# Kernel optimization log

Measured on AMD Instinct MI355X. Metric: run time of the kernel, lower is better.

Reference implementation:

```python
import jax, jax.numpy as jnp
from jax import lax
import numpy as np

H = 16        # hidden_size == input_size
L = 8         # num_layers


def _lstm_layer(x_seq, Wih, Whh, bih, bhh):
    # x_seq: [B, T, H] -> outputs [B, T, H]; PyTorch gate order i,f,g,o
    B = x_seq.shape[0]
    b = bih + bhh  # [4H]

    def step(carry, xt):
        h, c = carry
        gates = xt @ Wih.T + h @ Whh.T + b  # [B, 4H]
        i, f, g, o = jnp.split(gates, 4, axis=-1)
        c = jax.nn.sigmoid(f) * c + jax.nn.sigmoid(i) * jnp.tanh(g)
        h = jax.nn.sigmoid(o) * jnp.tanh(c)
        return (h, c), h

    h0 = jnp.zeros((B, H), x_seq.dtype)
    (_, _), hs = lax.scan(step, (h0, h0), jnp.swapaxes(x_seq, 0, 1))
    return jnp.swapaxes(hs, 0, 1)  # [B, T, H]


def setup_inputs() -> dict:
    key = jax.random.key(0)
    ks = jax.random.split(key, 9)
    s = 1.0 / np.sqrt(H)  # PyTorch default init scale
    x = jax.random.normal(ks[0], (2048, 512, H), dtype=jnp.float32)
    W_ih = jax.random.uniform(ks[1], (L, 4 * H, H), jnp.float32, -s, s)
    W_hh = jax.random.uniform(ks[2], (L, 4 * H, H), jnp.float32, -s, s)
    b_ih = jax.random.uniform(ks[3], (L, 4 * H), jnp.float32, -s, s)
    b_hh = jax.random.uniform(ks[4], (L, 4 * H), jnp.float32, -s, s)
    Wp = jax.random.uniform(ks[5], (3, H), jnp.float32, -s, s)
    bp = jax.random.uniform(ks[6], (3,), jnp.float32, -s, s)
    Wo = jax.random.uniform(ks[7], (3, H), jnp.float32, -s, s)
    bo = jax.random.uniform(ks[8], (3,), jnp.float32, -s, s)
    return {"x": x, "W_ih": W_ih, "W_hh": W_hh, "b_ih": b_ih, "b_hh": b_hh,
            "Wp": Wp, "bp": bp, "Wo": Wo, "bo": bo}


def reference(x, W_ih, W_hh, b_ih, b_hh, Wp, bp, Wo, bo):
    h = x
    for l in range(L):  # fixed small layer count
        h = _lstm_layer(h, W_ih[l], W_hh[l], b_ih[l], b_hh[l])
    last = h[:, -1, :]                       # [B, H]
    position = last @ Wp.T + bp              # [B, 3]
    orientation = jnp.tanh(last @ Wo.T + bo) # [B, 3]
    return jnp.concatenate((position, orientation), axis=1)  # [B, 6]
```

## Files before the change

### kernel.cpp

```cpp
#include <hip/hip_runtime.h>
#include <math.h>

typedef _Float16 f16x4 __attribute__((ext_vector_type(4)));
typedef _Float16 f16x2 __attribute__((ext_vector_type(2)));
typedef float    f32x4 __attribute__((ext_vector_type(4)));

constexpr int kT      = 512;
constexpr int kH      = 16;
constexpr int kL      = 8;
constexpr int kNB     = 8;
constexpr int kC      = 16;
constexpr int kChunks = kT / kC;
constexpr int kStages = kChunks + kL - 1;
constexpr int kRowE   = kNB * kH;

constexpr float kL2E = 1.4426950408889634f;

__device__ __forceinline__ float ex2(float w)  { return __builtin_amdgcn_exp2f(w); }
__device__ __forceinline__ float rcpf(float e) { return __builtin_amdgcn_rcpf(e); }

__global__ __launch_bounds__(512, 2)
void lstm_ck(const float* __restrict__ x,
             const float* __restrict__ Wih, const float* __restrict__ Whh,
             const float* __restrict__ bih, const float* __restrict__ bhh,
             const float* __restrict__ Wp,  const float* __restrict__ bpos,
             const float* __restrict__ Wo,  const float* __restrict__ bori,
             float* __restrict__ out)
{
    const int tid  = threadIdx.x;
    const int l    = tid >> 6;
    const int lane = tid & 63;
    const int n    = lane & 15;
    const int q    = lane >> 4;
    const int b    = n & 7;
    const int hi   = n >> 3;

    __shared__ __align__(16) _Float16 hbuf[2][kL - 1][kC][kNB][kH];
    __shared__ __align__(16) _Float16 headb[kNB][kH];

    const float asc = ((n & 3) == 2) ? (-2.0f * kL2E) : (-kL2E);
    f16x4 A1[4], A2[4];
    f32x4 bias[4];
    #pragma unroll
    for (int p = 0; p < 4; ++p) {
        const int wrow = (n & 3) * 16 + 4 * (n >> 2) + p;
        const float* w1 = Wih + (size_t)l * 64 * kH + wrow * kH + 4 * q;
        const float* w2 = Whh + (size_t)l * 64 * kH + wrow * kH + 4 * q;
        #pragma unroll
        for (int jj = 0; jj < 4; ++jj) {
            A1[p][jj] = (_Float16)(asc * w1[jj]);
            A2[p][jj] = (_Float16)(asc * w2[jj]);
        }
        #pragma unroll
        for (int r = 0; r < 4; ++r) {
            const float sc = (r == 2) ? (-2.0f * kL2E) : (-kL2E);
            const int g0 = l * 64 + r * 16 + 4 * q + p;
            bias[p][r] = sc * (bih[g0] + bhh[g0]);
        }
    }

    const float* xg = x + ((size_t)(blockIdx.x * kNB + b) * kT) * kH + 4 * q;
    f32x4 xf[kC];
    if (l == 0) {
        #pragma unroll
        for (int j = 0; j < kC; ++j)
            xf[j] = *(const f32x4*)(xg + (size_t)j * kH);
    }

    f16x4 B2r = { (_Float16)0.f, (_Float16)0.f, (_Float16)0.f, (_Float16)0.f };
    float cA = 0.f, cB = 0.f;

    #pragma unroll 1
    for (int s = 0; s < kStages; ++s) {
        const int c = s - l;
        if ((unsigned)c < (unsigned)kChunks) {
            f16x4 B1f[kC];
            if (l == 0) {
                #pragma unroll
                for (int j = 0; j < kC; ++j) {
                    f16x4 v = { (_Float16)xf[j][0], (_Float16)xf[j][1],
                                (_Float16)xf[j][2], (_Float16)xf[j][3] };
                    B1f[j] = v;
                }
                if (c + 1 < kChunks) {
                    #pragma unroll
                    for (int j = 0; j < kC; ++j)
                        xf[j] = *(const f32x4*)(xg + (size_t)((c + 1) * kC + j) * kH);
                }
            } else {
                const _Float16* src = &hbuf[c & 1][l - 1][0][b][4 * q];
                #pragma unroll
                for (int j = 0; j < kC; ++j)
                    B1f[j] = *(const f16x4*)(src + j * kRowE);
            }

            _Float16* wdst = &hbuf[c & 1][(l < kL - 1) ? l : 0][0][b][4 * q + 2 * hi];

            #pragma unroll
            for (int j = 0; j < kC; ++j) {
                f32x4 dIn0 = __builtin_amdgcn_mfma_f32_16x16x16f16(A1[0], B1f[j], bias[0], 0, 0, 0);
                f32x4 dIn1 = __builtin_amdgcn_mfma_f32_16x16x16f16(A1[1], B1f[j], bias[1], 0, 0, 0);
                f32x4 dIn2 = __builtin_amdgcn_mfma_f32_16x16x16f16(A1[2], B1f[j], bias[2], 0, 0, 0);
                f32x4 dIn3 = __builtin_amdgcn_mfma_f32_16x16x16f16(A1[3], B1f[j], bias[3], 0, 0, 0);
                f32x4 d0 = __builtin_amdgcn_mfma_f32_16x16x16f16(A2[0], B2r, dIn0, 0, 0, 0);
                f32x4 d1 = __builtin_amdgcn_mfma_f32_16x16x16f16(A2[1], B2r, dIn1, 0, 0, 0);
                f32x4 d2 = __builtin_amdgcn_mfma_f32_16x16x16f16(A2[2], B2r, dIn2, 0, 0, 0);
                f32x4 d3 = __builtin_amdgcn_mfma_f32_16x16x16f16(A2[3], B2r, dIn3, 0, 0, 0);

                f32x4 dA, dB;
                #pragma unroll
                for (int r = 0; r < 4; ++r) {
                    dA[r] = hi ? d2[r] : d0[r];
                    dB[r] = hi ? d3[r] : d1[r];
                }

                float hAf, hBf;
                {
                    const float Ei = ex2(fminf(dA[0], 40.0f));
                    const float Ef = ex2(fminf(dA[1], 40.0f));
                    const float Eg = ex2(fminf(dA[2], 40.0f));
                    const float Eo = ex2(fminf(dA[3], 60.0f));
                    const float Dg = 1.0f + Eg;
                    const float Df = 1.0f + Ef;
                    const float P1  = fmaf(Ei, Dg, Dg);
                    const float den = Df * P1;
                    const float t2  = fmaf(-Eg, Df, Df);
                    const float num = fmaf(cA, P1, t2);
                    const float cn  = num * rcpf(den);
                    cA = cn;
                    const float ac = fminf(cn * (-2.0f * kL2E), 60.0f);
                    const float Ec = ex2(ac);
                    const float Do = 1.0f + Eo;
                    const float R2 = rcpf(fmaf(Do, Ec, Do));
                    hAf = fmaf(-Ec, R2, R2);
                }
                {
                    const float Ei = ex2(fminf(dB[0], 40.0f));
                    const float Ef = ex2(fminf(dB[1], 40.0f));
                    const float Eg = ex2(fminf(dB[2], 40.0f));
                    const float Eo = ex2(fminf(dB[3], 60.0f));
                    const float Dg = 1.0f + Eg;
                    const float Df = 1.0f + Ef;
                    const float P1  = fmaf(Ei, Dg, Dg);
                    const float den = Df * P1;
                    const float t2  = fmaf(-Eg, Df, Df);
                    const float num = fmaf(cB, P1, t2);
                    const float cn  = num * rcpf(den);
                    cB = cn;
                    const float ac = fminf(cn * (-2.0f * kL2E), 60.0f);
                    const float Ec = ex2(ac);
                    const float Do = 1.0f + Eo;
                    const float R2 = rcpf(fmaf(Do, Ec, Do));
                    hBf = fmaf(-Ec, R2, R2);
                }

                f16x2 hp = { (_Float16)hAf, (_Float16)hBf };
                union { f16x2 h; int i; } uh; uh.h = hp;
                const int own   = uh.i;
                const int other = __shfl_xor(own, 8, 64);
                union { int i2[2]; f16x4 v; } ub;
                ub.i2[0] = hi ? other : own;
                ub.i2[1] = hi ? own : other;
                B2r = ub.v;

                if (l < kL - 1)
                    *(f16x2*)(wdst + j * kRowE) = hp;
                if (l == kL - 1 && c == kChunks - 1 && j == kC - 1)
                    *(f16x2*)(&headb[b][4 * q + 2 * hi]) = hp;
            }
        }
        asm volatile("s_waitcnt lgkmcnt(0)\n\ts_barrier" ::: "memory");
    }

    __syncthreads();

    if (l == kL - 1) {
        const int bb = lane >> 3;
        const int r  = lane & 7;
        if (r < 6) {
            const bool  isP   = (r < 3);
            const float* wrow = isP ? (Wp + r * kH) : (Wo + (r - 3) * kH);
            float acc = isP ? bpos[r] : bori[r - 3];
            #pragma unroll
            for (int u = 0; u < kH; ++u)
                acc = fmaf((float)headb[bb][u], wrow[u], acc);
            if (!isP) {
                const float Et = ex2(-2.0f * kL2E * acc);
                acc = fmaf(2.0f, rcpf(1.0f + Et), -1.0f);
            }
            out[(size_t)(blockIdx.x * kNB + bb) * 6 + r] = acc;
        }
    }
}

extern "C" void kernel_launch(void* const* d_in, const int* in_sizes, int n_in,
                              void* d_out, int out_size, void* d_ws, size_t ws_size,
                              hipStream_t stream) {
    const float* x    = (const float*)d_in[0];
    const float* Wih  = (const float*)d_in[1];
    const float* Whh  = (const float*)d_in[2];
    const float* bih  = (const float*)d_in[3];
    const float* bhh  = (const float*)d_in[4];
    const float* Wp   = (const float*)d_in[5];
    const float* bpos = (const float*)d_in[6];
    const float* Wo   = (const float*)d_in[7];
    const float* bori = (const float*)d_in[8];
    float* out = (float*)d_out;

    const int B = in_sizes[0] / (kT * kH);
    lstm_ck<<<dim3(B / kNB), dim3(512), 0, stream>>>(x, Wih, Whh, bih, bhh,
                                                     Wp, bpos, Wo, bori, out);
}
```

Measured before the change: 308.2 us.

## Halve batch per block so each lane computes one hidden unit, doubling blocks

```diff
diff --git a/kernel.cpp b/kernel.cpp
--- a/kernel.cpp
+++ b/kernel.cpp
@@ -2,13 +2,13 @@
 #include <math.h>
 
 typedef _Float16 f16x4 __attribute__((ext_vector_type(4)));
-typedef _Float16 f16x2 __attribute__((ext_vector_type(2)));
 typedef float    f32x4 __attribute__((ext_vector_type(4)));
+typedef float    f32x2 __attribute__((ext_vector_type(2)));
 
 constexpr int kT      = 512;
 constexpr int kH      = 16;
 constexpr int kL      = 8;
-constexpr int kNB     = 8;
+constexpr int kNB     = 4;
 constexpr int kC      = 16;
 constexpr int kChunks = kT / kC;
 constexpr int kStages = kChunks + kL - 1;
@@ -19,21 +19,23 @@
 __device__ __forceinline__ float ex2(float w)  { return __builtin_amdgcn_exp2f(w); }
 __device__ __forceinline__ float rcpf(float e) { return __builtin_amdgcn_rcpf(e); }
 
-__global__ __launch_bounds__(512, 2)
-void lstm_ck(const float* __restrict__ x,
-             const float* __restrict__ Wih, const float* __restrict__ Whh,
-             const float* __restrict__ bih, const float* __restrict__ bhh,
-             const float* __restrict__ Wp,  const float* __restrict__ bpos,
-             const float* __restrict__ Wo,  const float* __restrict__ bori,
-             float* __restrict__ out)
+__global__ __launch_bounds__(512, 4)
+void lstm_ck4(const float* __restrict__ x,
+              const float* __restrict__ Wih, const float* __restrict__ Whh,
+              const float* __restrict__ bih, const float* __restrict__ bhh,
+              const float* __restrict__ Wp,  const float* __restrict__ bpos,
+              const float* __restrict__ Wo,  const float* __restrict__ bori,
+              float* __restrict__ out)
 {
     const int tid  = threadIdx.x;
     const int l    = tid >> 6;
     const int lane = tid & 63;
     const int n    = lane & 15;
     const int q    = lane >> 4;
-    const int b    = n & 7;
-    const int hi   = n >> 3;
+    const int b    = n & 3;
+    const int t4   = n >> 2;
+    const int p2   = t4 >> 1;
+    const int myU  = 4 * q + t4;
 
     __shared__ __align__(16) _Float16 hbuf[2][kL - 1][kC][kNB][kH];
     __shared__ __align__(16) _Float16 headb[kNB][kH];
@@ -59,122 +61,114 @@
         }
     }
 
-    const float* xg = x + ((size_t)(blockIdx.x * kNB + b) * kT) * kH + 4 * q;
-    f32x4 xf[kC];
+    const float* xg = x + ((size_t)(blockIdx.x * kNB + b) * kT) * kH
+                        + 4 * q + 2 * p2;
+    f32x2 xf[kC];
     if (l == 0) {
         #pragma unroll
         for (int j = 0; j < kC; ++j)
-            xf[j] = *(const f32x4*)(xg + (size_t)j * kH);
+            xf[j] = *(const f32x2*)(xg + (size_t)j * kH);
     }
 
     f16x4 B2r = { (_Float16)0.f, (_Float16)0.f, (_Float16)0.f, (_Float16)0.f };
-    float cA = 0.f, cB = 0.f;
+    float c0 = 0.f;
 
     #pragma unroll 1
     for (int s = 0; s < kStages; ++s) {
         const int c = s - l;
         if ((unsigned)c < (unsigned)kChunks) {
-            f16x4 B1f[kC];
-            if (l == 0) {
-                #pragma unroll
-                for (int j = 0; j < kC; ++j) {
-                    f16x4 v = { (_Float16)xf[j][0], (_Float16)xf[j][1],
-                                (_Float16)xf[j][2], (_Float16)xf[j][3] };
-                    B1f[j] = v;
-                }
-                if (c + 1 < kChunks) {
-                    #pragma unroll
-                    for (int j = 0; j < kC; ++j)
-                        xf[j] = *(const f32x4*)(xg + (size_t)((c + 1) * kC + j) * kH);
-                }
-            } else {
-                const _Float16* src = &hbuf[c & 1][l - 1][0][b][4 * q];
-                #pragma unroll
-                for (int j = 0; j < kC; ++j)
-                    B1f[j] = *(const f16x4*)(src + j * kRowE);
-            }
-
-            _Float16* wdst = &hbuf[c & 1][(l < kL - 1) ? l : 0][0][b][4 * q + 2 * hi];
+            const _Float16* rsrc = &hbuf[c & 1][(l > 0) ? (l - 1) : 0][0][b][4 * q];
+            _Float16* wdst = &hbuf[c & 1][(l < kL - 1) ? l : 0][0][b][myU];
+
+            auto xB1 = [&](int j) -> f16x4 {
+                union { _Float16 h[2]; int i; } up;
+                up.h[0] = (_Float16)xf[j][0];
+                up.h[1] = (_Float16)xf[j][1];
+                const int pd = up.i;
+                const int od = __shfl_xor(pd, 8, 64);
+                union { int i2[2]; f16x4 v; } ua;
+                ua.i2[0] = p2 ? od : pd;
+                ua.i2[1] = p2 ? pd : od;
+                return ua.v;
+            };
+
+            f16x4 B1cur;
+            if (l > 0) B1cur = *(const f16x4*)(rsrc);
+            else       B1cur = xB1(0);
 
             #pragma unroll
             for (int j = 0; j < kC; ++j) {
-                f32x4 dIn0 = __builtin_amdgcn_mfma_f32_16x16x16f16(A1[0], B1f[j], bias[0], 0, 0, 0);
-                f32x4 dIn1 = __builtin_amdgcn_mfma_f32_16x16x16f16(A1[1], B1f[j], bias[1], 0, 0, 0);
-                f32x4 dIn2 = __builtin_amdgcn_mfma_f32_16x16x16f16(A1[2], B1f[j], bias[2], 0, 0, 0);
-                f32x4 dIn3 = __builtin_amdgcn_mfma_f32_16x16x16f16(A1[3], B1f[j], bias[3], 0, 0, 0);
+                f16x4 B1nxt;
+                if (j < kC - 1) {
+                    if (l > 0) B1nxt = *(const f16x4*)(rsrc + (j + 1) * kRowE);
+                    else       B1nxt = xB1(j + 1);
+                }
+
+                f32x4 dIn0 = __builtin_amdgcn_mfma_f32_16x16x16f16(A1[0], B1cur, bias[0], 0, 0, 0);
+                f32x4 dIn1 = __builtin_amdgcn_mfma_f32_16x16x16f16(A1[1], B1cur, bias[1], 0, 0, 0);
+                f32x4 dIn2 = __builtin_amdgcn_mfma_f32_16x16x16f16(A1[2], B1cur, bias[2], 0, 0, 0);
+                f32x4 dIn3 = __builtin_amdgcn_mfma_f32_16x16x16f16(A1[3], B1cur, bias[3], 0, 0, 0);
                 f32x4 d0 = __builtin_amdgcn_mfma_f32_16x16x16f16(A2[0], B2r, dIn0, 0, 0, 0);
                 f32x4 d1 = __builtin_amdgcn_mfma_f32_16x16x16f16(A2[1], B2r, dIn1, 0, 0, 0);
                 f32x4 d2 = __builtin_amdgcn_mfma_f32_16x16x16f16(A2[2], B2r, dIn2, 0, 0, 0);
                 f32x4 d3 = __builtin_amdgcn_mfma_f32_16x16x16f16(A2[3], B2r, dIn3, 0, 0, 0);
 
-                f32x4 dA, dB;
+                f32x4 d;
                 #pragma unroll
                 for (int r = 0; r < 4; ++r) {
-                    dA[r] = hi ? d2[r] : d0[r];
-                    dB[r] = hi ? d3[r] : d1[r];
+                    const float lo = (t4 & 1) ? d1[r] : d0[r];
+                    const float hi = (t4 & 1) ? d3[r] : d2[r];
+                    d[r] = (t4 & 2) ? hi : lo;
                 }
 
-                float hAf, hBf;
-                {
-                    const float Ei = ex2(fminf(dA[0], 40.0f));
-                    const float Ef = ex2(fminf(dA[1], 40.0f));
-                    const float Eg = ex2(fminf(dA[2], 40.0f));
-                    const float Eo = ex2(fminf(dA[3], 60.0f));
-                    const float Dg = 1.0f + Eg;
-                    const float Df = 1.0f + Ef;
-                    const float P1  = fmaf(Ei, Dg, Dg);
-                    const float den = Df * P1;
-                    const float t2  = fmaf(-Eg, Df, Df);
-                    const float num = fmaf(cA, P1, t2);
-                    const float cn  = num * rcpf(den);
-                    cA = cn;
-                    const float ac = fminf(cn * (-2.0f * kL2E), 60.0f);
-                    const float Ec = ex2(ac);
-                    const float Do = 1.0f + Eo;
-                    const float R2 = rcpf(fmaf(Do, Ec, Do));
-                    hAf = fmaf(-Ec, R2, R2);
-                }
-                {
-                    const float Ei = ex2(fminf(dB[0], 40.0f));
-                    const float Ef = ex2(fminf(dB[1], 40.0f));
-                    const float Eg = ex2(fminf(dB[2], 40.0f));
-                    const float Eo = ex2(fminf(dB[3], 60.0f));
-                    const float Dg = 1.0f + Eg;
-                    const float Df = 1.0f + Ef;
-                    const float P1  = fmaf(Ei, Dg, Dg);
-                    const float den = Df * P1;
-                    const float t2  = fmaf(-Eg, Df, Df);
-                    const float num = fmaf(cB, P1, t2);
-                    const float cn  = num * rcpf(den);
-                    cB = cn;
-                    const float ac = fminf(cn * (-2.0f * kL2E), 60.0f);
-                    const float Ec = ex2(ac);
-                    const float Do = 1.0f + Eo;
-                    const float R2 = rcpf(fmaf(Do, Ec, Do));
-                    hBf = fmaf(-Ec, R2, R2);
-                }
-
-                f16x2 hp = { (_Float16)hAf, (_Float16)hBf };
-                union { f16x2 h; int i; } uh; uh.h = hp;
-                const int own   = uh.i;
-                const int other = __shfl_xor(own, 8, 64);
+                const float Ei = ex2(fminf(d[0], 40.0f));
+                const float Ef = ex2(fminf(d[1], 40.0f));
+                const float Eg = ex2(fminf(d[2], 40.0f));
+                const float Eo = ex2(fminf(d[3], 60.0f));
+                const float Dg = 1.0f + Eg;
+                const float Df = 1.0f + Ef;
+                const float P1  = fmaf(Ei, Dg, Dg);
+                const float den = Df * P1;
+                const float t2  = fmaf(-Eg, Df, Df);
+                const float num = fmaf(c0, P1, t2);
+                const float cn  = num * rcpf(den);
+                c0 = cn;
+                const float ac = fminf(cn * (-2.0f * kL2E), 60.0f);
+                const float Ec = ex2(ac);
+                const float Do = 1.0f + Eo;
+                const float R2 = rcpf(fmaf(Do, Ec, Do));
+                const float hf = fmaf(-Ec, R2, R2);
+
+                const _Float16 h16 = (_Float16)hf;
+
+                if (l < kL - 1) wdst[j * kRowE] = h16;
+                else if (c == kChunks - 1 && j == kC - 1) headb[b][myU] = h16;
+
+                const int o16 = (int)(unsigned)__builtin_bit_cast(unsigned short, h16);
+                const int pp  = __shfl_xor(o16, 4, 64);
+                const int pairD = (t4 & 1) ? ((pp & 0xffff) | (o16 << 16))
+                                           : (o16 | (pp << 16));
+                const int othD  = __shfl_xor(pairD, 8, 64);
                 union { int i2[2]; f16x4 v; } ub;
-                ub.i2[0] = hi ? other : own;
-                ub.i2[1] = hi ? own : other;
+                ub.i2[0] = p2 ? othD : pairD;
+                ub.i2[1] = p2 ? pairD : othD;
                 B2r = ub.v;
 
-                if (l < kL - 1)
-                    *(f16x2*)(wdst + j * kRowE) = hp;
-                if (l == kL - 1 && c == kChunks - 1 && j == kC - 1)
-                    *(f16x2*)(&headb[b][4 * q + 2 * hi]) = hp;
+                if (j < kC - 1) B1cur = B1nxt;
             }
+
+            if (l == 0 && c + 1 < kChunks) {
+                #pragma unroll
+                for (int j = 0; j < kC; ++j)
+                    xf[j] = *(const f32x2*)(xg + (size_t)((c + 1) * kC + j) * kH);
+            }
         }
         asm volatile("s_waitcnt lgkmcnt(0)\n\ts_barrier" ::: "memory");
     }
 
     __syncthreads();
 
-    if (l == kL - 1) {
+    if (l == kL - 1 && lane < 32) {
         const int bb = lane >> 3;
         const int r  = lane & 7;
         if (r < 6) {
@@ -208,6 +202,6 @@
     float* out = (float*)d_out;
 
     const int B = in_sizes[0] / (kT * kH);
-    lstm_ck<<<dim3(B / kNB), dim3(512), 0, stream>>>(x, Wih, Whh, bih, bhh,
-                                                     Wp, bpos, Wo, bori, out);
+    lstm_ck4<<<dim3(B / kNB), dim3(512), 0, stream>>>(x, Wih, Whh, bih, bhh,
+                                                      Wp, bpos, Wo, bori, out);
 }
```

Result: slower. 375.4 us (+21.8%).
